# Optimization experiments

Hardware: AMD Instinct MI355X
Metric: run time of the kernel (lower is better)

Reference implementation:

```python
import jax, jax.numpy as jnp
import numpy as np
import math

EMBED_DIM = 64
NUM_HEADS = 4
HEAD_DIM = EMBED_DIM // NUM_HEADS
TGT = 64
SRC = 64
BSZ = 128


def setup_inputs() -> dict:
    key = jax.random.key(0)
    ks = jax.random.split(key, 8)
    x = jax.random.normal(ks[0], (TGT, BSZ, EMBED_DIM), dtype=jnp.float32)
    relation = jax.random.normal(ks[1], (TGT, SRC, BSZ, EMBED_DIM), dtype=jnp.float32)
    in_proj_weight = jax.random.normal(ks[2], (3 * EMBED_DIM, EMBED_DIM), dtype=jnp.float32) * 0.02
    in_proj_bias = jnp.zeros((3 * EMBED_DIM,), dtype=jnp.float32)
    rel_weight = jax.random.normal(ks[3], (2 * EMBED_DIM, EMBED_DIM), dtype=jnp.float32) * 0.02
    rel_bias = jnp.zeros((2 * EMBED_DIM,), dtype=jnp.float32)
    out_weight = jax.random.normal(ks[4], (EMBED_DIM, EMBED_DIM), dtype=jnp.float32) * 0.02
    out_bias = jnp.zeros((EMBED_DIM,), dtype=jnp.float32)
    return {
        'query': x, 'key': x, 'value': x, 'relation': relation,
        'in_proj_weight': in_proj_weight, 'in_proj_bias': in_proj_bias,
        'rel_weight': rel_weight, 'rel_bias': rel_bias,
        'out_weight': out_weight, 'out_bias': out_bias,
    }


def reference(query, key, value, relation, in_proj_weight, in_proj_bias,
              rel_weight, rel_bias, out_weight, out_bias):
    E, H, hd = EMBED_DIM, NUM_HEADS, HEAD_DIM
    t, b, _ = query.shape
    s = key.shape[0]
    scaling = hd ** (-0.5)
    # qkv projections (slices of the fused in_proj weight, as in _in_proj)
    q = query @ in_proj_weight[:E].T + in_proj_bias[:E]
    k = key @ in_proj_weight[E:2 * E].T + in_proj_bias[E:2 * E]
    v = value @ in_proj_weight[2 * E:].T + in_proj_bias[2 * E:]
    q = q.reshape(t, b * H, hd)
    k = k.reshape(s, b * H, hd)
    v = v.reshape(s, b * H, hd)
    # relation projection -> ra, rb, each [t, s, b*H, hd], then transpose(0,1)
    rel = relation @ rel_weight.T + rel_bias  # [t, s, b, 2E]
    ra = rel[..., :E].reshape(t, s, b * H, hd).swapaxes(0, 1)  # [s, t, bH, hd]
    rb = rel[..., E:].reshape(t, s, b * H, hd).swapaxes(0, 1)
    # q[i,j] = q[i] + ra_t[i,j]; requires t == s (broadcast as in torch)
    qp = (q[:, None] + ra) * scaling            # [t, s, bH, hd]
    kp = k[None, :] + rb                        # [t, s, bH, hd]
    attn_weights = jnp.einsum('ijbn,ijbn->ijb', qp, kp) * (1.0 / math.sqrt(hd))
    attn_weights = jax.nn.softmax(attn_weights, axis=1)
    attn = jnp.einsum('ijb,jbn->bin', attn_weights, v)  # [bH, t, hd]
    attn = attn.swapaxes(0, 1).reshape(t, b, E)
    out = attn @ out_weight.T + out_bias
    return out
```

## Files before the change

### kernel.cpp

```cpp
#include <hip/hip_runtime.h>
#include <hip/hip_bf16.h>

#define T_ 64
#define S_ 64
#define B_ 128
#define E_ 64
#define H_ 4

typedef float f32x4 __attribute__((ext_vector_type(4)));
typedef short bf16x8 __attribute__((ext_vector_type(8)));

static __device__ __forceinline__ short f2b(float f) {
    union { __hip_bfloat16 h; short s; } u;
    u.h = __float2bfloat16(f);
    return u.s;
}

__global__ __launch_bounds__(256) void k_qkv(
    const float* __restrict__ qin, const float* __restrict__ kin,
    const float* __restrict__ vin, const float* __restrict__ W,
    const float* __restrict__ bias, float* __restrict__ qkv)
{
    __shared__ float xs[3][32 * 68];
    __shared__ float WTs[64 * 68];
    const int tid = threadIdx.x;
    const int row0 = blockIdx.x * 32;

    #pragma unroll
    for (int l = 0; l < 6; ++l) {
        int f4 = l * 256 + tid;
        int src = f4 >> 9, rem = f4 & 511;
        int r = rem >> 4, e0 = (rem & 15) << 2;
        const float* xin = (src == 0) ? qin : (src == 1 ? kin : vin);
        float4 xv = reinterpret_cast<const float4*>(xin)[(size_t)(row0 + r) * 16 + (e0 >> 2)];
        float* dst = &xs[src][r * 68];
        dst[e0] = xv.x; dst[e0 + 1] = xv.y; dst[e0 + 2] = xv.z; dst[e0 + 3] = xv.w;
    }

    const int rq = tid >> 5, og = tid & 31;
    const int r0 = rq * 4, op0 = og * 2;

    for (int seg = 0; seg < 3; ++seg) {
        __syncthreads();
        #pragma unroll
        for (int l = 0; l < 4; ++l) {
            int f4 = l * 256 + tid;
            int o = f4 >> 4, e0 = (f4 & 15) << 2;
            float4 wv = reinterpret_cast<const float4*>(W)[(size_t)(seg * 64 + o) * 16 + (e0 >> 2)];
            WTs[(e0 + 0) * 68 + o] = wv.x; WTs[(e0 + 1) * 68 + o] = wv.y;
            WTs[(e0 + 2) * 68 + o] = wv.z; WTs[(e0 + 3) * 68 + o] = wv.w;
        }
        __syncthreads();

        float acc[4][2];
        #pragma unroll
        for (int rr = 0; rr < 4; ++rr) {
            acc[rr][0] = bias[seg * 64 + op0];
            acc[rr][1] = bias[seg * 64 + op0 + 1];
        }
        const float* xsrc = xs[seg];
        #pragma unroll 4
        for (int e = 0; e < 64; ++e) {
            float w0 = WTs[e * 68 + op0];
            float w1 = WTs[e * 68 + op0 + 1];
            #pragma unroll
            for (int rr = 0; rr < 4; ++rr) {
                float xv = xsrc[(r0 + rr) * 68 + e];
                acc[rr][0] += xv * w0;
                acc[rr][1] += xv * w1;
            }
        }
        #pragma unroll
        for (int rr = 0; rr < 4; ++rr) {
            float2 ov = make_float2(acc[rr][0], acc[rr][1]);
            reinterpret_cast<float2*>(
                &qkv[((size_t)seg * T_ * B_ + row0 + r0 + rr) * E_ + op0])[0] = ov;
        }
    }
}

__global__ __launch_bounds__(512, 4) void k_logits_mfma(
    const float* __restrict__ rel, const float* __restrict__ relW,
    const float* __restrict__ relBias, const float* __restrict__ qkv,
    float* __restrict__ logits)
{
    __shared__ char  Bs[16384];
    __shared__ float As[2][128 * 64];

    const int tid = threadIdx.x;
    const int w   = tid >> 6;
    const int l   = tid & 63;
    const int c   = l & 15;
    const int rq  = l >> 4;
    const int i   = blockIdx.x >> 3;
    const int jb  = (blockIdx.x & 7) * 8;

    #pragma unroll
    for (int li = 0; li < 4; ++li) {
        int f4 = li * 512 + tid;
        int o = f4 >> 4, e4 = f4 & 15;
        float4 wv = reinterpret_cast<const float4*>(relW)[f4];
        ushort4 bv;
        bv.x = (ushort)f2b(wv.x); bv.y = (ushort)f2b(wv.y);
        bv.z = (ushort)f2b(wv.z); bv.w = (ushort)f2b(wv.w);
        int ot = o >> 4, cc = o & 15;
        int ks = e4 >> 3, rqb = (e4 & 7) >> 1, half = e4 & 1;
        int dest = (ot * 2 + ks) * 1024 + (rqb * 16 + cc) * 16 + half * 8;
        *reinterpret_cast<ushort4*>(Bs + dest) = bv;
    }

    float qpre[4][4], bbv[4];
    {
        const float* qrow = qkv + (size_t)i * (B_ * E_);
        #pragma unroll
        for (int h = 0; h < 4; ++h) {
            float ba = relBias[h * 16 + c];
            bbv[h] = relBias[64 + h * 16 + c];
            #pragma unroll
            for (int r = 0; r < 4; ++r) {
                int b = w * 16 + rq * 4 + r;
                qpre[h][r] = qrow[b * E_ + h * 16 + c] + ba;
            }
        }
    }
    __syncthreads();

#define STAGE(jj, bufi)                                                        \
    {                                                                          \
        const char* srcb = (const char*)(rel + ((size_t)(jj) * S_ + i) * (size_t)(B_ * E_)); \
        char* dstb = (char*)&As[bufi][0] + w * 4096;                           \
        _Pragma("unroll")                                                      \
        for (int it = 0; it < 4; ++it) {                                       \
            int row = w * 16 + it * 4 + (l >> 4);                              \
            int srcoff = row * 256 + (((l & 15) ^ (row & 7)) << 4);            \
            __builtin_amdgcn_global_load_lds(                                  \
                (const __attribute__((address_space(1))) void*)(srcb + srcoff),\
                (__attribute__((address_space(3))) void*)(dstb + it * 1024),   \
                16, 0, 0);                                                     \
        }                                                                      \
    }

    float lbuf[8];
    int buf = 0;
    STAGE(jb, 0);

    #pragma unroll 1
    for (int t = 0; t < 8; ++t) {
        if (t < 7) {
            STAGE(jb + t + 1, buf ^ 1);
            asm volatile("s_waitcnt vmcnt(4) lgkmcnt(0)" ::: "memory");
        } else {
            asm volatile("s_waitcnt vmcnt(0) lgkmcnt(0)" ::: "memory");
        }
        const int j = jb + t;

        float kvv[4][4];
        {
            const float* krow = qkv + ((size_t)(T_ * B_) + (size_t)j * B_) * E_;
            #pragma unroll
            for (int h = 0; h < 4; ++h)
                #pragma unroll
                for (int r = 0; r < 4; ++r)
                    kvv[h][r] = krow[(w * 16 + rq * 4 + r) * E_ + h * 16 + c];
        }

        bf16x8 af[2];
        {
            const int row = w * 16 + c;
            const char* abase = (const char*)&As[buf][0] + row * 256;
            const int s7 = c & 7;
            #pragma unroll
            for (int ks = 0; ks < 2; ++ks) {
                float4 x0 = *(const float4*)(abase + (((ks * 8 + rq * 2 + 0) ^ s7) << 4));
                float4 x1 = *(const float4*)(abase + (((ks * 8 + rq * 2 + 1) ^ s7) << 4));
                bf16x8 a;
                a[0] = f2b(x0.x); a[1] = f2b(x0.y); a[2] = f2b(x0.z); a[3] = f2b(x0.w);
                a[4] = f2b(x1.x); a[5] = f2b(x1.y); a[6] = f2b(x1.z); a[7] = f2b(x1.w);
                af[ks] = a;
            }
        }

        f32x4 acc[8];
        #pragma unroll
        for (int ot = 0; ot < 8; ++ot) acc[ot] = (f32x4){0.f, 0.f, 0.f, 0.f};
        #pragma unroll
        for (int ot = 0; ot < 8; ++ot) {
            #pragma unroll
            for (int ks = 0; ks < 2; ++ks) {
                bf16x8 bfr = *(const bf16x8*)(Bs + (ot * 2 + ks) * 1024 + l * 16);
                acc[ot] = __builtin_amdgcn_mfma_f32_16x16x32_bf16(af[ks], bfr, acc[ot], 0, 0, 0);
            }
        }

        float v[16];
        #pragma unroll
        for (int h = 0; h < 4; ++h)
            #pragma unroll
            for (int r = 0; r < 4; ++r)
                v[h * 4 + r] = (qpre[h][r] + acc[h][r]) *
                               (kvv[h][r] + bbv[h] + acc[4 + h][r]);
        #pragma unroll
        for (int k = 0; k < 8; ++k) {
            float x = (c & 1) ? v[2 * k + 1] : v[2 * k];
            float y = (c & 1) ? v[2 * k] : v[2 * k + 1];
            v[k] = x + __shfl_xor(y, 1);
        }
        #pragma unroll
        for (int k = 0; k < 4; ++k) {
            float x = (c & 2) ? v[2 * k + 1] : v[2 * k];
            float y = (c & 2) ? v[2 * k] : v[2 * k + 1];
            v[k] = x + __shfl_xor(y, 2);
        }
        #pragma unroll
        for (int k = 0; k < 2; ++k) {
            float x = (c & 4) ? v[2 * k + 1] : v[2 * k];
            float y = (c & 4) ? v[2 * k] : v[2 * k + 1];
            v[k] = x + __shfl_xor(y, 4);
        }
        {
            float x = (c & 8) ? v[1] : v[0];
            float y = (c & 8) ? v[0] : v[1];
            lbuf[t] = (x + __shfl_xor(y, 8)) * 0.0625f;
        }
        buf ^= 1;
    }
#undef STAGE

    {
        const int hh = c >> 2, rr = c & 3;
        const int b = w * 16 + rq * 4 + rr;
        float* dst = &logits[(((size_t)i * B_ + b) * H_ + hh) * S_ + jb];
        *reinterpret_cast<float4*>(dst) = make_float4(lbuf[0], lbuf[1], lbuf[2], lbuf[3]);
        *reinterpret_cast<float4*>(dst + 4) = make_float4(lbuf[4], lbuf[5], lbuf[6], lbuf[7]);
    }
}

__global__ __launch_bounds__(256) void k_attn(
    const float* __restrict__ logits, const float* __restrict__ qkv,
    const float* __restrict__ Wout, const float* __restrict__ bout,
    float* __restrict__ out)
{
    __shared__ float wsm[4][H_][S_];
    __shared__ float ap[4][68];
    const int tid = threadIdx.x;
    const int i = blockIdx.x >> 5;
    const int bq = blockIdx.x & 31;
    const int w = tid >> 6, l = tid & 63;
    const int b = bq * 4 + w;

    const float* lg = logits + ((size_t)i * B_ + b) * H_ * S_;
    const int h = l >> 4, sub = l & 15;
    float v0 = lg[h * S_ + sub];
    float v1 = lg[h * S_ + sub + 16];
    float v2 = lg[h * S_ + sub + 32];
    float v3 = lg[h * S_ + sub + 48];
    float m = fmaxf(fmaxf(v0, v1), fmaxf(v2, v3));
    #pragma unroll
    for (int d = 1; d < 16; d <<= 1) m = fmaxf(m, __shfl_xor(m, d));
    float e0 = expf(v0 - m), e1 = expf(v1 - m), e2 = expf(v2 - m), e3 = expf(v3 - m);
    float ss = e0 + e1 + e2 + e3;
    #pragma unroll
    for (int d = 1; d < 16; d <<= 1) ss += __shfl_xor(ss, d);
    float inv = 1.0f / ss;
    wsm[w][h][sub] = e0 * inv;
    wsm[w][h][sub + 16] = e1 * inv;
    wsm[w][h][sub + 32] = e2 * inv;
    wsm[w][h][sub + 48] = e3 * inv;
    __syncthreads();

    const float* vbase = qkv + (size_t)2 * T_ * B_ * E_ + (size_t)b * E_;
    const float* wrow = &wsm[w][l >> 4][0];
    float acc = 0.f;
    #pragma unroll 4
    for (int j = 0; j < S_; ++j) acc += wrow[j] * vbase[(size_t)j * B_ * E_ + l];
    ap[w][l] = acc;
    __syncthreads();

    const float* wo = Wout + l * E_;
    const float* apw = ap[w];
    float oacc = bout[l];
    #pragma unroll 4
    for (int e = 0; e < E_; ++e) oacc += apw[e] * wo[e];
    out[((size_t)i * B_ + b) * E_ + l] = oacc;
}

extern "C" void kernel_launch(void* const* d_in, const int* in_sizes, int n_in,
                              void* d_out, int out_size, void* d_ws, size_t ws_size,
                              hipStream_t stream)
{
    const float* qin = (const float*)d_in[0];
    const float* kin = (const float*)d_in[1];
    const float* vin = (const float*)d_in[2];
    const float* rel = (const float*)d_in[3];
    const float* ipw = (const float*)d_in[4];
    const float* ipb = (const float*)d_in[5];
    const float* rw  = (const float*)d_in[6];
    const float* rb  = (const float*)d_in[7];
    const float* ow  = (const float*)d_in[8];
    const float* obias = (const float*)d_in[9];

    float* qkv = (float*)d_ws;
    float* logits = qkv + 3 * T_ * B_ * E_;
    float* out = (float*)d_out;

    k_qkv<<<dim3(256), dim3(256), 0, stream>>>(qin, kin, vin, ipw, ipb, qkv);
    k_logits_mfma<<<dim3(512), dim3(512), 0, stream>>>(rel, rw, rb, qkv, logits);
    k_attn<<<dim3(2048), dim3(256), 0, stream>>>(logits, qkv, ow, obias, out);
}
```

Before: 71.32 us.

## Load relation A-fragments directly into registers instead of staging through LDS

```diff
diff --git a/kernel.cpp b/kernel.cpp
--- a/kernel.cpp
+++ b/kernel.cpp
@@ -84,8 +84,7 @@
     const float* __restrict__ relBias, const float* __restrict__ qkv,
     float* __restrict__ logits)
 {
-    __shared__ char  Bs[16384];
-    __shared__ float As[2][128 * 64];
+    __shared__ char Bs[16384];
 
     const int tid = threadIdx.x;
     const int w   = tid >> 6;
@@ -125,59 +124,50 @@
     }
     __syncthreads();
 
-#define STAGE(jj, bufi)                                                        \
-    {                                                                          \
-        const char* srcb = (const char*)(rel + ((size_t)(jj) * S_ + i) * (size_t)(B_ * E_)); \
-        char* dstb = (char*)&As[bufi][0] + w * 4096;                           \
-        _Pragma("unroll")                                                      \
-        for (int it = 0; it < 4; ++it) {                                       \
-            int row = w * 16 + it * 4 + (l >> 4);                              \
-            int srcoff = row * 256 + (((l & 15) ^ (row & 7)) << 4);            \
-            __builtin_amdgcn_global_load_lds(                                  \
-                (const __attribute__((address_space(1))) void*)(srcb + srcoff),\
-                (__attribute__((address_space(3))) void*)(dstb + it * 1024),   \
-                16, 0, 0);                                                     \
-        }                                                                      \
-    }
+    const int arow = ((w * 16 + c) * E_) + rq * 8;
+    const int kbase = (w * 16 + rq * 4) * E_;
 
     float lbuf[8];
-    int buf = 0;
-    STAGE(jb, 0);
+    float4 a0, a1, a2, a3;
+    {
+        const float* ab = rel + ((size_t)jb * S_ + i) * (size_t)(B_ * E_) + arow;
+        a0 = *(const float4*)(ab);
+        a1 = *(const float4*)(ab + 4);
+        a2 = *(const float4*)(ab + 32);
+        a3 = *(const float4*)(ab + 36);
+    }
 
     #pragma unroll 1
     for (int t = 0; t < 8; ++t) {
+        const int j = jb + t;
+
+        bf16x8 af[2];
+        {
+            bf16x8 a;
+            a[0] = f2b(a0.x); a[1] = f2b(a0.y); a[2] = f2b(a0.z); a[3] = f2b(a0.w);
+            a[4] = f2b(a1.x); a[5] = f2b(a1.y); a[6] = f2b(a1.z); a[7] = f2b(a1.w);
+            af[0] = a;
+            a[0] = f2b(a2.x); a[1] = f2b(a2.y); a[2] = f2b(a2.z); a[3] = f2b(a2.w);
+            a[4] = f2b(a3.x); a[5] = f2b(a3.y); a[6] = f2b(a3.z); a[7] = f2b(a3.w);
+            af[1] = a;
+        }
+
         if (t < 7) {
-            STAGE(jb + t + 1, buf ^ 1);
-            asm volatile("s_waitcnt vmcnt(4) lgkmcnt(0)" ::: "memory");
-        } else {
-            asm volatile("s_waitcnt vmcnt(0) lgkmcnt(0)" ::: "memory");
-        }
-        const int j = jb + t;
+            const float* ab = rel + ((size_t)(j + 1) * S_ + i) * (size_t)(B_ * E_) + arow;
+            a0 = *(const float4*)(ab);
+            a1 = *(const float4*)(ab + 4);
+            a2 = *(const float4*)(ab + 32);
+            a3 = *(const float4*)(ab + 36);
+        }
 
         float kvv[4][4];
         {
-            const float* krow = qkv + ((size_t)(T_ * B_) + (size_t)j * B_) * E_;
+            const float* krow = qkv + ((size_t)(T_ * B_) + (size_t)j * B_) * E_ + kbase;
             #pragma unroll
             for (int h = 0; h < 4; ++h)
                 #pragma unroll
                 for (int r = 0; r < 4; ++r)
-                    kvv[h][r] = krow[(w * 16 + rq * 4 + r) * E_ + h * 16 + c];
-        }
-
-        bf16x8 af[2];
-        {
-            const int row = w * 16 + c;
-            const char* abase = (const char*)&As[buf][0] + row * 256;
-            const int s7 = c & 7;
-            #pragma unroll
-            for (int ks = 0; ks < 2; ++ks) {
-                float4 x0 = *(const float4*)(abase + (((ks * 8 + rq * 2 + 0) ^ s7) << 4));
-                float4 x1 = *(const float4*)(abase + (((ks * 8 + rq * 2 + 1) ^ s7) << 4));
-                bf16x8 a;
-                a[0] = f2b(x0.x); a[1] = f2b(x0.y); a[2] = f2b(x0.z); a[3] = f2b(x0.w);
-                a[4] = f2b(x1.x); a[5] = f2b(x1.y); a[6] = f2b(x1.z); a[7] = f2b(x1.w);
-                af[ks] = a;
-            }
+                    kvv[h][r] = krow[r * E_ + h * 16 + c];
         }
 
         f32x4 acc[8];
@@ -222,9 +212,7 @@
             float y = (c & 8) ? v[0] : v[1];
             lbuf[t] = (x + __shfl_xor(y, 8)) * 0.0625f;
         }
-        buf ^= 1;
-    }
-#undef STAGE
+    }
 
     {
         const int hh = c >> 2, rr = c & 3;
```

Measured after the change: 137.8 us. 1.93x slower.
